# Performance work log

Measured on AMD Instinct MI355X. Metric: run time of the kernel, lower is better.

Reference implementation:

```python
import jax
import jax.numpy as jnp
import numpy as np

B, S, D, H, HID, E, TOPK = 1, 2048, 1024, 16, 4096, 8, 2
HEAD_DIM = D // H


def _layer_norm(x, g, b, eps=1e-5):
    mu = jnp.mean(x, axis=-1, keepdims=True)
    var = jnp.var(x, axis=-1, keepdims=True)
    return (x - mu) * jax.lax.rsqrt(var + eps) * g + b


def setup_inputs() -> dict:
    key = jax.random.key(0)
    ks = jax.random.split(key, 12)
    s = 0.02
    return {
        "x": jax.random.normal(ks[0], (B, S, D), jnp.float32),
        "ln1_g": jnp.ones((D,), jnp.float32),
        "ln1_b": jnp.zeros((D,), jnp.float32),
        "wq": jax.random.normal(ks[1], (D, D), jnp.float32) * s,
        "wk": jax.random.normal(ks[2], (D, D), jnp.float32) * s,
        "wv": jax.random.normal(ks[3], (D, D), jnp.float32) * s,
        "wo": jax.random.normal(ks[4], (D, D), jnp.float32) * s,
        "ln2_g": jnp.ones((D,), jnp.float32),
        "ln2_b": jnp.zeros((D,), jnp.float32),
        "w_gate": jax.random.normal(ks[5], (D, E), jnp.float32) * s,
        "w_eg": jax.random.normal(ks[6], (E, D, HID), jnp.float32) * s,
        "w_eu": jax.random.normal(ks[7], (E, D, HID), jnp.float32) * s,
        "w_ed": jax.random.normal(ks[8], (E, HID, D), jnp.float32) * s,
    }


def _attention(h, wq, wk, wv, wo):
    b, s, d = h.shape
    q = (h @ wq).reshape(b, s, H, HEAD_DIM).transpose(0, 2, 1, 3)
    k = (h @ wk).reshape(b, s, H, HEAD_DIM).transpose(0, 2, 1, 3)
    v = (h @ wv).reshape(b, s, H, HEAD_DIM).transpose(0, 2, 1, 3)
    scores = jnp.einsum("bhqd,bhkd->bhqk", q, k) / jnp.sqrt(jnp.asarray(HEAD_DIM, h.dtype))
    causal = jnp.tril(jnp.ones((s, s), bool))  # [s,s]
    scores = jnp.where(causal, scores, jnp.asarray(-1e30, h.dtype))
    attn = jax.nn.softmax(scores, axis=-1)
    out = jnp.einsum("bhqk,bhkd->bhqd", attn, v).transpose(0, 2, 1, 3).reshape(b, s, d)
    return out @ wo


def _moe(h, w_gate, w_eg, w_eu, w_ed):
    b, s, d = h.shape
    flat = h.reshape(-1, d)  # [T,D]
    logits = flat @ w_gate  # [T,E]
    scores = jax.nn.sigmoid(logits)
    top_val, top_idx = jax.lax.top_k(scores, TOPK)
    top_val = top_val / (jnp.sum(top_val, axis=-1, keepdims=True) + 1e-9)
    # per-token per-expert combine weight (0 for unrouted experts)
    combine = jnp.sum(jax.nn.one_hot(top_idx, E, dtype=flat.dtype) * top_val[..., None], axis=1)  # [T,E]
    g = jax.nn.silu(jnp.einsum("td,edh->eth", flat, w_eg))
    u = jnp.einsum("td,edh->eth", flat, w_eu)
    eo = jnp.einsum("eth,ehd->etd", g * u, w_ed)  # [E,T,D]
    out = jnp.einsum("etd,te->td", eo, combine)
    return out.reshape(b, s, d)


def reference(x, ln1_g, ln1_b, wq, wk, wv, wo, ln2_g, ln2_b, w_gate, w_eg, w_eu, w_ed):
    x = x + _attention(_layer_norm(x, ln1_g, ln1_b), wq, wk, wv, wo)
    x = x + _moe(_layer_norm(x, ln2_g, ln2_b), w_gate, w_eg, w_eu, w_ed)
    return x
```

## Files before the change

### kernel.cpp

```cpp
#include <hip/hip_runtime.h>
#include <hip/hip_bf16.h>
#include <stdint.h>

#define DI __device__ __forceinline__

typedef short bf16x8_t __attribute__((ext_vector_type(8)));
typedef float f32x4_t __attribute__((ext_vector_type(4)));

DI unsigned short f2bf(float f) {
  __hip_bfloat16 h = __float2bfloat16(f);
  unsigned short u;
  __builtin_memcpy(&u, &h, 2);
  return u;
}

DI uint32_t pk2(float a, float b) {
  return (uint32_t)f2bf(a) | ((uint32_t)f2bf(b) << 16);
}

DI f32x4_t mfma16(bf16x8_t a, bf16x8_t b, f32x4_t c) {
  return __builtin_amdgcn_mfma_f32_16x16x32_bf16(a, b, c, 0, 0, 0);
}

DI void gload16(const void* g, void* l) {
  __builtin_amdgcn_global_load_lds(
      (const __attribute__((address_space(1))) uint32_t*)g,
      (__attribute__((address_space(3))) uint32_t*)l, 16, 0, 0);
}

DI bf16x8_t frag(const unsigned short* base, int row, int hi) {
  return *(const bf16x8_t*)&base[row * 32 + ((hi ^ ((row >> 1) & 3)) * 8)];
}
DI int chunk_swz(int tid) { return ((tid & 3) ^ ((tid >> 3) & 3)) * 8; }

__global__ __launch_bounds__(256) void transpose_cvt4(const float* __restrict__ s0, const float* __restrict__ s1,
                                                      const float* __restrict__ s2, const float* __restrict__ s3,
                                                      unsigned short* __restrict__ d0, unsigned short* __restrict__ d1,
                                                      unsigned short* __restrict__ d2, unsigned short* __restrict__ d3) {
  __shared__ float tile[64][65];
  const int z = blockIdx.z;
  const float* in = (z == 0) ? s0 : (z == 1) ? s1 : (z == 2) ? s2 : s3;
  unsigned short* out = (z == 0) ? d0 : (z == 1) ? d1 : (z == 2) ? d2 : d3;
  const int tid = threadIdx.x;
  const int tx = tid & 15, ty = tid >> 4;
  const int r0 = blockIdx.y * 64, c0 = blockIdx.x * 64;
#pragma unroll
  for (int i = 0; i < 4; ++i) {
    const int r = ty + i * 16;
    const float4 v = *(const float4*)(in + (size_t)(r0 + r) * 1024 + c0 + tx * 4);
    tile[r][tx * 4 + 0] = v.x; tile[r][tx * 4 + 1] = v.y;
    tile[r][tx * 4 + 2] = v.z; tile[r][tx * 4 + 3] = v.w;
  }
  __syncthreads();
#pragma unroll
  for (int i = 0; i < 4; ++i) {
    const int r = ty + i * 16;
    ushort4 o;
    o.x = f2bf(tile[tx * 4 + 0][r]); o.y = f2bf(tile[tx * 4 + 1][r]);
    o.z = f2bf(tile[tx * 4 + 2][r]); o.w = f2bf(tile[tx * 4 + 3][r]);
    *(ushort4*)(out + (size_t)(c0 + r) * 1024 + r0 + tx * 4) = o;
  }
}

__global__ __launch_bounds__(256) void ln_kernel(const float* __restrict__ x, const float* __restrict__ g,
                                                 const float* __restrict__ b, unsigned short* __restrict__ out) {
  const int row = blockIdx.x, tid = threadIdx.x;
  const int wid = tid >> 6, lane = tid & 63;
  const float4 v = *(const float4*)(x + (size_t)row * 1024 + tid * 4);
  float s = v.x + v.y + v.z + v.w;
  float s2 = v.x * v.x + v.y * v.y + v.z * v.z + v.w * v.w;
#pragma unroll
  for (int o = 1; o < 64; o <<= 1) { s += __shfl_xor(s, o); s2 += __shfl_xor(s2, o); }
  __shared__ float red[8];
  if (lane == 0) { red[wid] = s; red[4 + wid] = s2; }
  __syncthreads();
  const float ts = red[0] + red[1] + red[2] + red[3];
  const float ts2 = red[4] + red[5] + red[6] + red[7];
  const float mu = ts * 0.0009765625f;
  const float var = ts2 * 0.0009765625f - mu * mu;
  const float rs = rsqrtf(var + 1e-5f);
  const float4 gg = *(const float4*)(g + tid * 4);
  const float4 bb = *(const float4*)(b + tid * 4);
  ushort4 o4;
  o4.x = f2bf((v.x - mu) * rs * gg.x + bb.x);
  o4.y = f2bf((v.y - mu) * rs * gg.y + bb.y);
  o4.z = f2bf((v.z - mu) * rs * gg.z + bb.z);
  o4.w = f2bf((v.w - mu) * rs * gg.w + bb.w);
  *(ushort4*)(out + (size_t)row * 1024 + tid * 4) = o4;
}

template<int BN>
DI void gemm_loop(const unsigned short* aR0, const unsigned short* aR1,
                  const unsigned short* bR0, const unsigned short* bR1,
                  const int K, unsigned short* lds, const int tid,
                  f32x4_t (&acc)[4][BN / 32]) {
  constexpr int NF = BN / 32;
  unsigned short* ldsA = lds;
  unsigned short* ldsB = lds + 4096;
  const int wid = tid >> 6, lane = tid & 63, ln = lane & 15, hi = lane >> 4;
  const int wr = wid >> 1, wc = wid & 1;
  char* dstA0 = (char*)ldsA + wid * 1024;
  char* dstA1 = (char*)ldsA + 4096 + wid * 1024;
  char* dstB0 = (char*)ldsB + wid * 1024;
  char* dstB1 = (char*)ldsB + 4096 + wid * 1024;
  for (int k0 = 0; k0 < K; k0 += 32) {
    gload16(aR0 + k0, dstA0);
    gload16(aR1 + k0, dstA1);
    gload16(bR0 + k0, dstB0);
    if constexpr (BN == 128) gload16(bR1 + k0, dstB1);
    __syncthreads();
    bf16x8_t af[4];
#pragma unroll
    for (int mf = 0; mf < 4; ++mf)
      af[mf] = frag(ldsA, wr * 64 + mf * 16 + ln, hi);
    __builtin_amdgcn_s_setprio(1);
#pragma unroll
    for (int nf = 0; nf < NF; ++nf) {
      bf16x8_t bfr = frag(ldsB, wc * (BN / 2) + nf * 16 + ln, hi);
#pragma unroll
      for (int mf = 0; mf < 4; ++mf)
        acc[mf][nf] = mfma16(af[mf], bfr, acc[mf][nf]);
    }
    __builtin_amdgcn_s_setprio(0);
    __syncthreads();
  }
}

__global__ __launch_bounds__(256) void qkv_kernel(const unsigned short* __restrict__ h1,
                                                  const unsigned short* __restrict__ wqT,
                                                  const unsigned short* __restrict__ wkT,
                                                  const unsigned short* __restrict__ wvT,
                                                  unsigned short* __restrict__ qb,
                                                  unsigned short* __restrict__ kbf,
                                                  unsigned short* __restrict__ vt) {
  __shared__ unsigned short lds[128 * 32 + 128 * 32];
  const int tid = threadIdx.x;
  const int z = blockIdx.z;
  const unsigned short* BT = (z == 0) ? wqT : (z == 1) ? wkT : wvT;
  const int m0 = blockIdx.y * 128, n0 = blockIdx.x * 128;
  f32x4_t acc[4][4] = {};
  const int cs = chunk_swz(tid);
  const unsigned short* aR0 = h1 + (size_t)(m0 + (tid >> 2)) * 1024 + cs;
  const unsigned short* aR1 = aR0 + 64 * 1024;
  const unsigned short* bR0 = BT + (size_t)(n0 + (tid >> 2)) * 1024 + cs;
  const unsigned short* bR1 = bR0 + 64 * 1024;
  gemm_loop<128>(aR0, aR1, bR0, bR1, 1024, lds, tid, acc);
  const int lane = tid & 63, ln = lane & 15, hi = lane >> 4, wid = tid >> 6;
  const int wr = wid >> 1, wc = wid & 1;
  if (z < 2) {
    unsigned short* o = z ? kbf : qb;
#pragma unroll
    for (int mf = 0; mf < 4; ++mf)
#pragma unroll
      for (int nf = 0; nf < 4; ++nf)
#pragma unroll
        for (int r = 0; r < 4; ++r) {
          const int m = m0 + wr * 64 + mf * 16 + hi * 4 + r;
          const int n = n0 + wc * 64 + nf * 16 + ln;
          o[(size_t)m * 1024 + n] = f2bf(acc[mf][nf][r]);
        }
  } else {
#pragma unroll
    for (int mf = 0; mf < 4; ++mf)
#pragma unroll
      for (int nf = 0; nf < 4; ++nf) {
        const int n = n0 + wc * 64 + nf * 16 + ln;
        const int mb = m0 + wr * 64 + mf * 16 + hi * 4;
        ushort4 o;
        o.x = f2bf(acc[mf][nf][0]); o.y = f2bf(acc[mf][nf][1]);
        o.z = f2bf(acc[mf][nf][2]); o.w = f2bf(acc[mf][nf][3]);
        *(ushort4*)(vt + (size_t)n * 2048 + mb) = o;
      }
  }
}

__global__ __launch_bounds__(256) void wo_kernel(const unsigned short* __restrict__ ao,
                                                 const unsigned short* __restrict__ woT,
                                                 const float* __restrict__ x,
                                                 float* __restrict__ out) {
  __shared__ unsigned short lds[128 * 32 + 64 * 32];
  const int tid = threadIdx.x;
  const int m0 = blockIdx.y * 128, n0 = blockIdx.x * 64;
  f32x4_t acc[4][2] = {};
  const int cs = chunk_swz(tid);
  const unsigned short* aR0 = ao + (size_t)(m0 + (tid >> 2)) * 1024 + cs;
  const unsigned short* aR1 = aR0 + 64 * 1024;
  const unsigned short* bR0 = woT + (size_t)(n0 + (tid >> 2)) * 1024 + cs;
  gemm_loop<64>(aR0, aR1, bR0, nullptr, 1024, lds, tid, acc);
  const int lane = tid & 63, ln = lane & 15, hi = lane >> 4, wid = tid >> 6;
  const int wr = wid >> 1, wc = wid & 1;
#pragma unroll
  for (int mf = 0; mf < 4; ++mf)
#pragma unroll
    for (int nf = 0; nf < 2; ++nf)
#pragma unroll
      for (int r = 0; r < 4; ++r) {
        const int m = m0 + wr * 64 + mf * 16 + hi * 4 + r;
        const int n = n0 + wc * 32 + nf * 16 + ln;
        out[(size_t)m * 1024 + n] = acc[mf][nf][r] + x[(size_t)m * 1024 + n];
      }
}

__global__ __launch_bounds__(256) void attn_kernel(const unsigned short* __restrict__ qb,
                                                   const unsigned short* __restrict__ kbuf,
                                                   const unsigned short* __restrict__ vt,
                                                   unsigned short* __restrict__ ao) {
  __shared__ unsigned short kTl[4096];
  __shared__ unsigned short vTl[4096];
  __shared__ unsigned short pl[4][1024];
  const int tid = threadIdx.x;
  const int wid = tid >> 6, lane = tid & 63;
  const int ln = lane & 15, hi = lane >> 4;
  const int h = blockIdx.y;
  const int qi = (h < 8) ? blockIdx.x : (31 - blockIdx.x);
  const int q0 = qi * 64;
  const int q0w = q0 + wid * 16;

  const unsigned short* qrow = qb + (size_t)(q0w + ln) * 1024 + h * 64 + hi * 8;
  const bf16x8_t aq0 = *(const bf16x8_t*)(qrow);
  const bf16x8_t aq1 = *(const bf16x8_t*)(qrow + 32);

  const int str_r = tid >> 3, str_c = tid & 7;
  const int swc = (str_c ^ (str_r & 7)) * 8;
  const unsigned short* ksrc0 = kbuf + (size_t)str_r * 1024 + h * 64 + swc;
  const unsigned short* ksrc1 = kbuf + (size_t)(str_r + 32) * 1024 + h * 64 + swc;
  const unsigned short* vsrc0 = vt + (size_t)(h * 64 + str_r) * 2048 + swc;
  const unsigned short* vsrc1 = vt + (size_t)(h * 64 + str_r + 32) * 2048 + swc;
  char* kd0 = (char*)kTl + wid * 1024;
  char* kd1 = (char*)kTl + 4096 + wid * 1024;
  char* vd0 = (char*)vTl + wid * 1024;
  char* vd1 = (char*)vTl + 4096 + wid * 1024;

  float m_r[4], l_r[4];
  f32x4_t o_acc[4] = {};
#pragma unroll
  for (int r = 0; r < 4; ++r) { m_r[r] = -1e30f; l_r[r] = 0.f; }

  const int nkv = qi + 1;
  for (int it = 0; it < nkv; ++it) {
    const int kv0 = it * 64;
    gload16(ksrc0 + (size_t)kv0 * 1024, kd0);
    gload16(ksrc1 + (size_t)kv0 * 1024, kd1);
    gload16(vsrc0 + kv0, vd0);
    gload16(vsrc1 + kv0, vd1);
    __syncthreads();

    float sc[4][4];
    __builtin_amdgcn_s_setprio(1);
#pragma unroll
    for (int cf = 0; cf < 4; ++cf) {
      const int row = cf * 16 + ln;
      const int swz = row & 7;
      const bf16x8_t b0 = *(const bf16x8_t*)((char*)kTl + row * 128 + ((hi ^ swz) * 16));
      const bf16x8_t b1 = *(const bf16x8_t*)((char*)kTl + row * 128 + (((4 + hi) ^ swz) * 16));
      f32x4_t zacc = {};
      zacc = mfma16(aq0, b0, zacc);
      zacc = mfma16(aq1, b1, zacc);
#pragma unroll
      for (int r = 0; r < 4; ++r) sc[cf][r] = zacc[r] * 0.125f;
    }
    __builtin_amdgcn_s_setprio(0);
    if (kv0 + 63 > q0w) {
#pragma unroll
      for (int cf = 0; cf < 4; ++cf)
#pragma unroll
        for (int r = 0; r < 4; ++r) {
          const int qg = q0w + hi * 4 + r;
          const int kg = kv0 + cf * 16 + ln;
          if (kg > qg) sc[cf][r] = -1e30f;
        }
    }
#pragma unroll
    for (int r = 0; r < 4; ++r) {
      float tm = fmaxf(fmaxf(sc[0][r], sc[1][r]), fmaxf(sc[2][r], sc[3][r]));
      tm = fmaxf(tm, __shfl_xor(tm, 1));
      tm = fmaxf(tm, __shfl_xor(tm, 2));
      tm = fmaxf(tm, __shfl_xor(tm, 4));
      tm = fmaxf(tm, __shfl_xor(tm, 8));
      const float mn = fmaxf(m_r[r], tm);
      const float alpha = __expf(m_r[r] - mn);
      float rsum = 0.f;
#pragma unroll
      for (int cf = 0; cf < 4; ++cf) {
        const float p = __expf(sc[cf][r] - mn);
        sc[cf][r] = p; rsum += p;
      }
      rsum += __shfl_xor(rsum, 1); rsum += __shfl_xor(rsum, 2);
      rsum += __shfl_xor(rsum, 4); rsum += __shfl_xor(rsum, 8);
      l_r[r] = l_r[r] * alpha + rsum;
      m_r[r] = mn;
#pragma unroll
      for (int df = 0; df < 4; ++df) o_acc[df][r] *= alpha;
    }
    unsigned short* pw = &pl[wid][0];
#pragma unroll
    for (int cf = 0; cf < 4; ++cf)
#pragma unroll
      for (int r = 0; r < 4; ++r) {
        const int qq = hi * 4 + r;
        const int kv = cf * 16 + ln;
        const int bo = (qq * 128 + kv * 2) ^ ((qq & 7) << 4);
        *(unsigned short*)((char*)pw + bo) = f2bf(sc[cf][r]);
      }
    asm volatile("s_waitcnt lgkmcnt(0)" ::: "memory");
    __builtin_amdgcn_sched_barrier(0);
    const bf16x8_t pa0 = *(const bf16x8_t*)((char*)pw + ((ln * 128 + hi * 16) ^ ((ln & 7) << 4)));
    const bf16x8_t pa1 = *(const bf16x8_t*)((char*)pw + ((ln * 128 + 64 + hi * 16) ^ ((ln & 7) << 4)));
    __builtin_amdgcn_s_setprio(1);
#pragma unroll
    for (int df = 0; df < 4; ++df) {
      const int d = df * 16 + ln;
      const int swz = d & 7;
      const bf16x8_t bv0 = *(const bf16x8_t*)((char*)vTl + d * 128 + ((hi ^ swz) * 16));
      const bf16x8_t bv1 = *(const bf16x8_t*)((char*)vTl + d * 128 + (((4 + hi) ^ swz) * 16));
      o_acc[df] = mfma16(pa0, bv0, o_acc[df]);
      o_acc[df] = mfma16(pa1, bv1, o_acc[df]);
    }
    __builtin_amdgcn_s_setprio(0);
    __syncthreads();
  }
#pragma unroll
  for (int df = 0; df < 4; ++df) {
    const int n = h * 64 + df * 16 + ln;
#pragma unroll
    for (int r = 0; r < 4; ++r) {
      const int m = q0w + hi * 4 + r;
      ao[(size_t)m * 1024 + n] = f2bf(o_acc[df][r] / l_r[r]);
    }
  }
}

__global__ __launch_bounds__(256) void gate_kernel(const float* __restrict__ x2, const float* __restrict__ g,
                                                   const float* __restrict__ b, const float* __restrict__ wg,
                                                   unsigned short* __restrict__ h2o,
                                                   int2* __restrict__ te, float2* __restrict__ tw,
                                                   int* __restrict__ cnt) {
  const int tid = threadIdx.x, wid = tid >> 6, lane = tid & 63;
  const int t = blockIdx.x * 4 + wid;
  const float* row = x2 + (size_t)t * 1024;
  float vv[16];
#pragma unroll
  for (int i = 0; i < 4; ++i) *(float4*)&vv[i * 4] = *(const float4*)(row + lane * 16 + i * 4);
  float s = 0.f, s2 = 0.f;
#pragma unroll
  for (int j = 0; j < 16; ++j) { s += vv[j]; s2 += vv[j] * vv[j]; }
#pragma unroll
  for (int o = 1; o < 64; o <<= 1) { s += __shfl_xor(s, o); s2 += __shfl_xor(s2, o); }
  const float mu = s * 0.0009765625f;
  const float var = s2 * 0.0009765625f - mu * mu;
  const float rs = rsqrtf(var + 1e-5f);
  float acc[8] = {0.f, 0.f, 0.f, 0.f, 0.f, 0.f, 0.f, 0.f};
  bf16x8_t o0, o1;
#pragma unroll
  for (int j = 0; j < 16; ++j) {
    const int d = lane * 16 + j;
    const float xv = (vv[j] - mu) * rs * g[d] + b[d];
    if (j < 8) o0[j] = (short)f2bf(xv); else o1[j - 8] = (short)f2bf(xv);
    const float4 w0 = *(const float4*)(wg + d * 8);
    const float4 w1 = *(const float4*)(wg + d * 8 + 4);
    acc[0] += xv * w0.x; acc[1] += xv * w0.y; acc[2] += xv * w0.z; acc[3] += xv * w0.w;
    acc[4] += xv * w1.x; acc[5] += xv * w1.y; acc[6] += xv * w1.z; acc[7] += xv * w1.w;
  }
  *(bf16x8_t*)(h2o + (size_t)t * 1024 + lane * 16) = o0;
  *(bf16x8_t*)(h2o + (size_t)t * 1024 + lane * 16 + 8) = o1;
#pragma unroll
  for (int o = 1; o < 64; o <<= 1) {
#pragma unroll
    for (int e = 0; e < 8; ++e) acc[e] += __shfl_xor(acc[e], o);
  }
  if (lane == 0) {
    float sg[8];
#pragma unroll
    for (int e = 0; e < 8; ++e) sg[e] = 1.f / (1.f + __expf(-acc[e]));
    int e0 = 0;
#pragma unroll
    for (int e = 1; e < 8; ++e) if (sg[e] > sg[e0]) e0 = e;
    int e1 = (e0 == 0) ? 1 : 0;
#pragma unroll
    for (int e = 0; e < 8; ++e) if (e != e0 && sg[e] > sg[e1]) e1 = e;
    const float v0 = sg[e0], v1 = sg[e1];
    const float inv = 1.f / (v0 + v1 + 1e-9f);
    te[t] = make_int2(e0, e1);
    tw[t] = make_float2(v0 * inv, v1 * inv);
    atomicAdd(&cnt[e0], 1);
    atomicAdd(&cnt[e1], 1);
  }
}

__global__ void zero_counters(int* p) { if (threadIdx.x < 8) p[threadIdx.x] = 0; }

__global__ __launch_bounds__(256) void g2_kernel(const int* __restrict__ cnt, int* __restrict__ slot_off,
                                                 int* __restrict__ tile_expert, int* __restrict__ tile_rowbase,
                                                 int* __restrict__ cursor, int* __restrict__ assign_token,
                                                 float* __restrict__ assign_w) {
  const int tid = threadIdx.x;
  for (int i = tid; i < 8192; i += 256) { assign_token[i] = -1; assign_w[i] = 0.f; }
  if (tid == 0) {
    int base = 0, tiles = 0;
    for (int e = 0; e < 8; ++e) {
      const int c = cnt[e];
      slot_off[e] = base;
      cursor[e] = 0;
      const int nt = (c + 255) >> 8;
      for (int i = 0; i < nt; ++i) {
        tile_expert[tiles] = e;
        tile_rowbase[tiles] = base + i * 256;
        ++tiles;
      }
      base += nt * 256;
    }
    for (; tiles < 40; ++tiles) tile_expert[tiles] = -1;
  }
}

__global__ __launch_bounds__(256) void g3_kernel(const int2* __restrict__ te, const float2* __restrict__ tw,
                                                 const int* __restrict__ slot_off, int* __restrict__ cursor,
                                                 int* __restrict__ assign_token, float* __restrict__ assign_w) {
  const int t = blockIdx.x * 256 + threadIdx.x;
  const int2 e = te[t];
  const float2 w = tw[t];
  const int s0 = slot_off[e.x] + atomicAdd(&cursor[e.x], 1);
  assign_token[s0] = t; assign_w[s0] = w.x;
  const int s1 = slot_off[e.y] + atomicAdd(&cursor[e.y], 1);
  assign_token[s1] = t; assign_w[s1] = w.y;
}

DI void stageA4(const unsigned short* a0, const unsigned short* a1,
                const unsigned short* a2, const unsigned short* a3,
                int koff, char* Ab, int wid) {
  gload16(a0 + koff, Ab + wid * 1024);
  gload16(a1 + koff, Ab + 4096 + wid * 1024);
  gload16(a2 + koff, Ab + 8192 + wid * 1024);
  gload16(a3 + koff, Ab + 12288 + wid * 1024);
}
DI void stageA2(const unsigned short* a0, const unsigned short* a1,
                int koff, char* Ab, int wid) {
  gload16(a0 + koff, Ab + wid * 1024);
  gload16(a1 + koff, Ab + 4096 + wid * 1024);
}

DI void ug_write_b(char* Bn, const int* boff, const float4& q0, const float4& q1,
                   const float4& q2, const float4& q3) {
  const float* q0p = (const float*)&q0; const float* q1p = (const float*)&q1;
  const float* q2p = (const float*)&q2; const float* q3p = (const float*)&q3;
#pragma unroll
  for (int i = 0; i < 4; ++i) {
    uint2 w;
    w.x = pk2(q0p[i], q1p[i]);
    w.y = pk2(q2p[i], q3p[i]);
    *(uint2*)(Bn + boff[i]) = w;
  }
}

DI void ug_mfma256(const unsigned short* A, const char* Bb, int wr, int wc, int ln, int hi,
                   f32x4_t (&accg)[8][2], f32x4_t (&accu)[8][2]) {
  bf16x8_t af[8];
#pragma unroll
  for (int mf = 0; mf < 8; ++mf)
    af[mf] = frag(A, wr * 128 + mf * 16 + ln, hi);
  __builtin_amdgcn_s_setprio(1);
#pragma unroll
  for (int nf = 0; nf < 2; ++nf) {
    const int nrow = wc * 32 + nf * 16 + ln;
    int bo = nrow * 64 + hi * 16;
    bo ^= ((nrow >> 2) & 7) << 4;
    const bf16x8_t bg = *(const bf16x8_t*)(Bb + bo);
    const bf16x8_t bu = *(const bf16x8_t*)(Bb + 4096 + bo);
#pragma unroll
    for (int mf = 0; mf < 8; ++mf) {
      accg[mf][nf] = mfma16(af[mf], bg, accg[mf][nf]);
      accu[mf][nf] = mfma16(af[mf], bu, accu[mf][nf]);
    }
  }
  __builtin_amdgcn_s_setprio(0);
}

__global__ __launch_bounds__(256, 2) void upgate_kernel(const unsigned short* __restrict__ h2,
                                                        const float* __restrict__ w_eg, const float* __restrict__ w_eu,
                                                        const int* __restrict__ tile_expert,
                                                        const int* __restrict__ tile_rowbase,
                                                        const int* __restrict__ assign_token,
                                                        unsigned short* __restrict__ act) {
  const int by = blockIdx.y;
  const int e = tile_expert[by];
  if (e < 0) return;
  const int n0 = blockIdx.x * 64;
  const int rowbase = tile_rowbase[by];
  const int tid = threadIdx.x;
  __shared__ unsigned short lds[2 * 8192 + 2 * 4096];
  char* A0 = (char*)lds;
  char* A1 = (char*)lds + 16384;
  char* B0 = (char*)lds + 32768;
  char* B1 = (char*)lds + 40960;
  const int wid = tid >> 6, lane = tid & 63, ln = lane & 15, hi = lane >> 4;
  const int wr = wid >> 1, wc = wid & 1;
  const int r0s = rowbase + (tid >> 2);
  int tk0 = assign_token[r0s];        tk0 = tk0 < 0 ? 0 : tk0;
  int tk1 = assign_token[r0s + 64];   tk1 = tk1 < 0 ? 0 : tk1;
  int tk2 = assign_token[r0s + 128];  tk2 = tk2 < 0 ? 0 : tk2;
  int tk3 = assign_token[r0s + 192];  tk3 = tk3 < 0 ? 0 : tk3;
  const int cs = chunk_swz(tid);
  const unsigned short* aR0 = h2 + (size_t)tk0 * 1024 + cs;
  const unsigned short* aR1 = h2 + (size_t)tk1 * 1024 + cs;
  const unsigned short* aR2 = h2 + (size_t)tk2 * 1024 + cs;
  const unsigned short* aR3 = h2 + (size_t)tk3 * 1024 + cs;
  const int mat = tid >> 7;
  const int blk = tid & 127;
  const int kb = (blk >> 4) * 4;
  const int nb = (blk & 15) * 4;
  const float* bsrc = (mat ? w_eu : w_eg) + (size_t)e * 1024 * 4096 + (size_t)kb * 4096 + n0 + nb;
  int boff[4];
#pragma unroll
  for (int i = 0; i < 4; ++i) {
    const int n = nb + i;
    int bo = mat * 4096 + n * 64 + kb * 2;
    bo ^= ((n >> 2) & 7) << 4;
    boff[i] = bo;
  }
  f32x4_t accg[8][2] = {};
  f32x4_t accu[8][2] = {};
  float4 qA0, qA1, qA2, qA3, qB0, qB1, qB2, qB3;
  stageA4(aR0, aR1, aR2, aR3, 0, A0, wid);
  qB0 = *(const float4*)(bsrc);
  qB1 = *(const float4*)(bsrc + 4096);
  qB2 = *(const float4*)(bsrc + 8192);
  qB3 = *(const float4*)(bsrc + 12288);
  __builtin_amdgcn_sched_barrier(0);
  ug_write_b(B0, boff, qB0, qB1, qB2, qB3);
  {
    const float* bs = bsrc + (size_t)32 * 4096;
    qA0 = *(const float4*)(bs);
    qA1 = *(const float4*)(bs + 4096);
    qA2 = *(const float4*)(bs + 8192);
    qA3 = *(const float4*)(bs + 12288);
  }
  asm volatile("s_waitcnt lgkmcnt(0)" ::: "memory");
  __builtin_amdgcn_sched_barrier(0);
  __builtin_amdgcn_s_barrier();
  for (int p = 0; p < 15; ++p) {
    {
      const int t = 2 * p;
      stageA4(aR0, aR1, aR2, aR3, (t + 1) * 32, A1, wid);
      const float* bs = bsrc + (size_t)(t + 2) * 32 * 4096;
      qB0 = *(const float4*)(bs);
      qB1 = *(const float4*)(bs + 4096);
      qB2 = *(const float4*)(bs + 8192);
      qB3 = *(const float4*)(bs + 12288);
      __builtin_amdgcn_sched_barrier(0);
      ug_write_b(B1, boff, qA0, qA1, qA2, qA3);
      ug_mfma256((const unsigned short*)A0, B0, wr, wc, ln, hi, accg, accu);
      asm volatile("s_waitcnt vmcnt(4)" ::: "memory");
      __builtin_amdgcn_sched_barrier(0);
      asm volatile("s_waitcnt lgkmcnt(0)" ::: "memory");
      __builtin_amdgcn_sched_barrier(0);
      __builtin_amdgcn_s_barrier();
    }
    {
      const int t = 2 * p + 1;
      stageA4(aR0, aR1, aR2, aR3, (t + 1) * 32, A0, wid);
      const float* bs = bsrc + (size_t)(t + 2) * 32 * 4096;
      qA0 = *(const float4*)(bs);
      qA1 = *(const float4*)(bs + 4096);
      qA2 = *(const float4*)(bs + 8192);
      qA3 = *(const float4*)(bs + 12288);
      __builtin_amdgcn_sched_barrier(0);
      ug_write_b(B0, boff, qB0, qB1, qB2, qB3);
      ug_mfma256((const unsigned short*)A1, B1, wr, wc, ln, hi, accg, accu);
      asm volatile("s_waitcnt vmcnt(4)" ::: "memory");
      __builtin_amdgcn_sched_barrier(0);
      asm volatile("s_waitcnt lgkmcnt(0)" ::: "memory");
      __builtin_amdgcn_sched_barrier(0);
      __builtin_amdgcn_s_barrier();
    }
  }
  stageA4(aR0, aR1, aR2, aR3, 31 * 32, A1, wid);
  __builtin_amdgcn_sched_barrier(0);
  ug_write_b(B1, boff, qA0, qA1, qA2, qA3);
  ug_mfma256((const unsigned short*)A0, B0, wr, wc, ln, hi, accg, accu);
  asm volatile("s_waitcnt vmcnt(0)" ::: "memory");
  __builtin_amdgcn_sched_barrier(0);
  asm volatile("s_waitcnt lgkmcnt(0)" ::: "memory");
  __builtin_amdgcn_sched_barrier(0);
  __builtin_amdgcn_s_barrier();
  ug_mfma256((const unsigned short*)A1, B1, wr, wc, ln, hi, accg, accu);
#pragma unroll
  for (int mf = 0; mf < 8; ++mf)
#pragma unroll
    for (int nf = 0; nf < 2; ++nf)
#pragma unroll
      for (int r = 0; r < 4; ++r) {
        const int m = wr * 128 + mf * 16 + hi * 4 + r;
        const int n = n0 + wc * 32 + nf * 16 + ln;
        const float gv = accg[mf][nf][r], uv = accu[mf][nf][r];
        const float val = gv / (1.f + __expf(-gv)) * uv;
        act[(size_t)(rowbase + m) * 4096 + n] = f2bf(val);
      }
}

DI void dn_write_b(char* Bn, const int* boff, const float4& q0, const float4& q1) {
  const float* q0p = (const float*)&q0; const float* q1p = (const float*)&q1;
#pragma unroll
  for (int i = 0; i < 4; ++i)
    *(uint32_t*)(Bn + boff[i]) = pk2(q0p[i], q1p[i]);
}

DI void dn_mfma(const unsigned short* A, const char* Bb, int wr, int wc, int ln, int hi,
                f32x4_t (&acc)[4][2]) {
  bf16x8_t af[4];
#pragma unroll
  for (int mf = 0; mf < 4; ++mf)
    af[mf] = frag(A, wr * 64 + mf * 16 + ln, hi);
  __builtin_amdgcn_s_setprio(1);
#pragma unroll
  for (int nf = 0; nf < 2; ++nf) {
    const int nrow = wc * 32 + nf * 16 + ln;
    int bo = nrow * 64 + hi * 16;
    bo ^= ((nrow >> 2) & 7) << 4;
    const bf16x8_t bb = *(const bf16x8_t*)(Bb + bo);
#pragma unroll
    for (int mf = 0; mf < 4; ++mf)
      acc[mf][nf] = mfma16(af[mf], bb, acc[mf][nf]);
  }
  __builtin_amdgcn_s_setprio(0);
}

__global__ __launch_bounds__(256) void down_kernel(const unsigned short* __restrict__ act,
                                                   const float* __restrict__ w_ed,
                                                   const int* __restrict__ tile_expert,
                                                   const int* __restrict__ tile_rowbase,
                                                   const int* __restrict__ assign_token,
                                                   const float* __restrict__ assign_w,
                                                   float* __restrict__ out) {
  const int tix = blockIdx.y;
  const int e = tile_expert[tix >> 1];
  if (e < 0) return;
  const int rowbase = tile_rowbase[tix >> 1] + (tix & 1) * 128;
  const int n0 = blockIdx.x * 64;
  const int kz = blockIdx.z * 1024;
  const int tid = threadIdx.x;
  __shared__ unsigned short lds[2 * 4096 + 2 * 2048];
  char* A0 = (char*)lds;
  char* A1 = (char*)lds + 8192;
  char* B0 = (char*)lds + 16384;
  char* B1 = (char*)lds + 20480;
  const int wid = tid >> 6, lane = tid & 63, ln = lane & 15, hi = lane >> 4;
  const int wr = wid >> 1, wc = wid & 1;
  const int cs = chunk_swz(tid);
  const unsigned short* aR0 = act + (size_t)(rowbase + (tid >> 2)) * 4096 + kz + cs;
  const unsigned short* aR1 = aR0 + (size_t)64 * 4096;
  const int nb = (tid & 15) * 4;
  const int kb2 = (tid >> 4) * 2;
  const float* bsrc = w_ed + (size_t)e * 4096 * 1024 + (size_t)(kz + kb2) * 1024 + n0 + nb;
  int boff[4];
#pragma unroll
  for (int i = 0; i < 4; ++i) {
    const int n = nb + i;
    int bo = n * 64 + kb2 * 2;
    bo ^= ((n >> 2) & 7) << 4;
    boff[i] = bo;
  }
  f32x4_t acc[4][2] = {};
  float4 qA0, qA1, qB0, qB1;
  stageA2(aR0, aR1, 0, A0, wid);
  qB0 = *(const float4*)(bsrc);
  qB1 = *(const float4*)(bsrc + 1024);
  __builtin_amdgcn_sched_barrier(0);
  dn_write_b(B0, boff, qB0, qB1);
  {
    const float* bs = bsrc + (size_t)32 * 1024;
    qA0 = *(const float4*)(bs);
    qA1 = *(const float4*)(bs + 1024);
  }
  asm volatile("s_waitcnt lgkmcnt(0)" ::: "memory");
  __builtin_amdgcn_sched_barrier(0);
  __builtin_amdgcn_s_barrier();
  for (int p = 0; p < 15; ++p) {
    {
      const int t = 2 * p;
      stageA2(aR0, aR1, (t + 1) * 32, A1, wid);
      const float* bs = bsrc + (size_t)(t + 2) * 32 * 1024;
      qB0 = *(const float4*)(bs);
      qB1 = *(const float4*)(bs + 1024);
      __builtin_amdgcn_sched_barrier(0);
      dn_write_b(B1, boff, qA0, qA1);
      dn_mfma((const unsigned short*)A0, B0, wr, wc, ln, hi, acc);
      asm volatile("s_waitcnt vmcnt(2)" ::: "memory");
      __builtin_amdgcn_sched_barrier(0);
      asm volatile("s_waitcnt lgkmcnt(0)" ::: "memory");
      __builtin_amdgcn_sched_barrier(0);
      __builtin_amdgcn_s_barrier();
    }
    {
      const int t = 2 * p + 1;
      stageA2(aR0, aR1, (t + 1) * 32, A0, wid);
      const float* bs = bsrc + (size_t)(t + 2) * 32 * 1024;
      qA0 = *(const float4*)(bs);
      qA1 = *(const float4*)(bs + 1024);
      __builtin_amdgcn_sched_barrier(0);
      dn_write_b(B0, boff, qB0, qB1);
      dn_mfma((const unsigned short*)A1, B1, wr, wc, ln, hi, acc);
      asm volatile("s_waitcnt vmcnt(2)" ::: "memory");
      __builtin_amdgcn_sched_barrier(0);
      asm volatile("s_waitcnt lgkmcnt(0)" ::: "memory");
      __builtin_amdgcn_sched_barrier(0);
      __builtin_amdgcn_s_barrier();
    }
  }
  stageA2(aR0, aR1, 31 * 32, A1, wid);
  __builtin_amdgcn_sched_barrier(0);
  dn_write_b(B1, boff, qA0, qA1);
  dn_mfma((const unsigned short*)A0, B0, wr, wc, ln, hi, acc);
  asm volatile("s_waitcnt vmcnt(0)" ::: "memory");
  __builtin_amdgcn_sched_barrier(0);
  asm volatile("s_waitcnt lgkmcnt(0)" ::: "memory");
  __builtin_amdgcn_sched_barrier(0);
  __builtin_amdgcn_s_barrier();
  dn_mfma((const unsigned short*)A1, B1, wr, wc, ln, hi, acc);
#pragma unroll
  for (int mf = 0; mf < 4; ++mf)
#pragma unroll
    for (int r = 0; r < 4; ++r) {
      const int m = wr * 64 + mf * 16 + hi * 4 + r;
      const int slot = rowbase + m;
      const int tk = assign_token[slot];
      if (tk >= 0) {
        const float w = assign_w[slot];
#pragma unroll
        for (int nf = 0; nf < 2; ++nf) {
          const int n = n0 + wc * 32 + nf * 16 + ln;
          atomicAdd(out + (size_t)tk * 1024 + n, acc[mf][nf][r] * w);
        }
      }
    }
}

extern "C" void kernel_launch(void* const* d_in, const int* in_sizes, int n_in,
                              void* d_out, int out_size, void* d_ws, size_t ws_size,
                              hipStream_t stream) {
  (void)in_sizes; (void)n_in; (void)out_size;
  const float* x    = (const float*)d_in[0];
  const float* ln1g = (const float*)d_in[1];
  const float* ln1b = (const float*)d_in[2];
  const float* wq   = (const float*)d_in[3];
  const float* wk   = (const float*)d_in[4];
  const float* wv   = (const float*)d_in[5];
  const float* wo   = (const float*)d_in[6];
  const float* ln2g = (const float*)d_in[7];
  const float* ln2b = (const float*)d_in[8];
  const float* wg   = (const float*)d_in[9];
  const float* weg  = (const float*)d_in[10];
  const float* weu  = (const float*)d_in[11];
  const float* wed  = (const float*)d_in[12];
  float* out = (float*)d_out;
  char* ws = (char*)d_ws;

  const size_t MB = (size_t)1 << 20;
  if (ws_size < 86 * MB) return;
  unsigned short* wqT = (unsigned short*)(ws + 0 * MB);
  unsigned short* wkT = (unsigned short*)(ws + 2 * MB);
  unsigned short* wvT = (unsigned short*)(ws + 4 * MB);
  unsigned short* woT = (unsigned short*)(ws + 6 * MB);
  unsigned short* h1  = (unsigned short*)(ws + 8 * MB);
  unsigned short* qb  = (unsigned short*)(ws + 12 * MB);
  unsigned short* kbf = (unsigned short*)(ws + 16 * MB);
  unsigned short* vt  = (unsigned short*)(ws + 20 * MB);
  unsigned short* ao  = (unsigned short*)(ws + 24 * MB);
  unsigned short* h2  = (unsigned short*)(ws + 28 * MB);
  unsigned short* act = (unsigned short*)(ws + 32 * MB);
  int2*   te = (int2*)(ws + 84 * MB);
  float2* tw = (float2*)(ws + 84 * MB + 16384);
  int*  meta = (int*)(ws + 84 * MB + 32768);
  int* cnt = meta;
  int* cursor = meta + 8;
  int* slot_off = meta + 16;
  int* tile_expert = meta + 24;
  int* tile_rowbase = meta + 64;
  int*   assign_token = (int*)(ws + 84 * MB + 36864);
  float* assign_w     = (float*)(ws + 84 * MB + 36864 + 32768);

  zero_counters<<<1, 64, 0, stream>>>(cnt);
  transpose_cvt4<<<dim3(16, 16, 4), 256, 0, stream>>>(wq, wk, wv, wo, wqT, wkT, wvT, woT);
  ln_kernel<<<2048, 256, 0, stream>>>(x, ln1g, ln1b, h1);
  qkv_kernel<<<dim3(8, 16, 3), 256, 0, stream>>>(h1, wqT, wkT, wvT, qb, kbf, vt);
  attn_kernel<<<dim3(32, 16), 256, 0, stream>>>(qb, kbf, vt, ao);
  wo_kernel<<<dim3(16, 16), 256, 0, stream>>>(ao, woT, x, out);
  gate_kernel<<<512, 256, 0, stream>>>(out, ln2g, ln2b, wg, h2, te, tw, cnt);
  g2_kernel<<<1, 256, 0, stream>>>(cnt, slot_off, tile_expert, tile_rowbase, cursor, assign_token, assign_w);
  g3_kernel<<<8, 256, 0, stream>>>(te, tw, slot_off, cursor, assign_token, assign_w);
  upgate_kernel<<<dim3(64, 24), 256, 0, stream>>>(h2, weg, weu, tile_expert, tile_rowbase, assign_token, act);
  down_kernel<<<dim3(16, 48, 4), 256, 0, stream>>>(act, wed, tile_expert, tile_rowbase, assign_token, assign_w, out);
}
```

Measured before the change: 481.2 us.

## Double-buffer LDS tiles in GEMM loop and attention KV loop

The GEMM main loop and the attention KV loop now use two LDS buffers. The next K-tile (or KV tile) is fetched from global memory while MFMAs run on the current one, and the barrier before compute is removed, leaving one barrier per iteration. The goal is to hide global-to-LDS load latency behind matrix math. The cost is double the LDS footprint per block, which can lower occupancy, especially for the attention kernel.

```diff
diff --git a/kernel.cpp b/kernel.cpp
--- a/kernel.cpp
+++ b/kernel.cpp
@@ -95,28 +95,40 @@
                   const int K, unsigned short* lds, const int tid,
                   f32x4_t (&acc)[4][BN / 32]) {
   constexpr int NF = BN / 32;
-  unsigned short* ldsA = lds;
-  unsigned short* ldsB = lds + 4096;
+  constexpr int BSZ = (BN == 128) ? 4096 : 2048;
   const int wid = tid >> 6, lane = tid & 63, ln = lane & 15, hi = lane >> 4;
   const int wr = wid >> 1, wc = wid & 1;
-  char* dstA0 = (char*)ldsA + wid * 1024;
-  char* dstA1 = (char*)ldsA + 4096 + wid * 1024;
-  char* dstB0 = (char*)ldsB + wid * 1024;
-  char* dstB1 = (char*)ldsB + 4096 + wid * 1024;
-  for (int k0 = 0; k0 < K; k0 += 32) {
-    gload16(aR0 + k0, dstA0);
-    gload16(aR1 + k0, dstA1);
-    gload16(bR0 + k0, dstB0);
-    if constexpr (BN == 128) gload16(bR1 + k0, dstB1);
-    __syncthreads();
+  const int nk = K >> 5;
+  {
+    char* Ab = (char*)lds;
+    char* Bb = (char*)lds + 16384;
+    gload16(aR0, Ab + wid * 1024);
+    gload16(aR1, Ab + 4096 + wid * 1024);
+    gload16(bR0, Bb + wid * 1024);
+    if constexpr (BN == 128) gload16(bR1, Bb + 4096 + wid * 1024);
+  }
+  __syncthreads();
+  for (int t = 0; t < nk; ++t) {
+    if (t + 1 < nk) {
+      const int k0 = (t + 1) << 5;
+      const int b = (t + 1) & 1;
+      char* Ab = (char*)lds + b * 8192;
+      char* Bb = (char*)lds + 16384 + b * (BSZ * 2);
+      gload16(aR0 + k0, Ab + wid * 1024);
+      gload16(aR1 + k0, Ab + 4096 + wid * 1024);
+      gload16(bR0 + k0, Bb + wid * 1024);
+      if constexpr (BN == 128) gload16(bR1 + k0, Bb + 4096 + wid * 1024);
+    }
+    const unsigned short* A = lds + (t & 1) * 4096;
+    const unsigned short* B = lds + 8192 + (t & 1) * BSZ;
     bf16x8_t af[4];
 #pragma unroll
     for (int mf = 0; mf < 4; ++mf)
-      af[mf] = frag(ldsA, wr * 64 + mf * 16 + ln, hi);
+      af[mf] = frag(A, wr * 64 + mf * 16 + ln, hi);
     __builtin_amdgcn_s_setprio(1);
 #pragma unroll
     for (int nf = 0; nf < NF; ++nf) {
-      bf16x8_t bfr = frag(ldsB, wc * (BN / 2) + nf * 16 + ln, hi);
+      bf16x8_t bfr = frag(B, wc * (BN / 2) + nf * 16 + ln, hi);
 #pragma unroll
       for (int mf = 0; mf < 4; ++mf)
         acc[mf][nf] = mfma16(af[mf], bfr, acc[mf][nf]);
@@ -133,7 +145,7 @@
                                                   unsigned short* __restrict__ qb,
                                                   unsigned short* __restrict__ kbf,
                                                   unsigned short* __restrict__ vt) {
-  __shared__ unsigned short lds[128 * 32 + 128 * 32];
+  __shared__ unsigned short lds[16384];
   const int tid = threadIdx.x;
   const int z = blockIdx.z;
   const unsigned short* BT = (z == 0) ? wqT : (z == 1) ? wkT : wvT;
@@ -178,7 +190,7 @@
                                                  const unsigned short* __restrict__ woT,
                                                  const float* __restrict__ x,
                                                  float* __restrict__ out) {
-  __shared__ unsigned short lds[128 * 32 + 64 * 32];
+  __shared__ unsigned short lds[12288];
   const int tid = threadIdx.x;
   const int m0 = blockIdx.y * 128, n0 = blockIdx.x * 64;
   f32x4_t acc[4][2] = {};
@@ -205,8 +217,8 @@
                                                    const unsigned short* __restrict__ kbuf,
                                                    const unsigned short* __restrict__ vt,
                                                    unsigned short* __restrict__ ao) {
-  __shared__ unsigned short kTl[4096];
-  __shared__ unsigned short vTl[4096];
+  __shared__ unsigned short kTl[8192];
+  __shared__ unsigned short vTl[8192];
   __shared__ unsigned short pl[4][1024];
   const int tid = threadIdx.x;
   const int wid = tid >> 6, lane = tid & 63;
@@ -226,10 +238,6 @@
   const unsigned short* ksrc1 = kbuf + (size_t)(str_r + 32) * 1024 + h * 64 + swc;
   const unsigned short* vsrc0 = vt + (size_t)(h * 64 + str_r) * 2048 + swc;
   const unsigned short* vsrc1 = vt + (size_t)(h * 64 + str_r + 32) * 2048 + swc;
-  char* kd0 = (char*)kTl + wid * 1024;
-  char* kd1 = (char*)kTl + 4096 + wid * 1024;
-  char* vd0 = (char*)vTl + wid * 1024;
-  char* vd1 = (char*)vTl + 4096 + wid * 1024;
 
   float m_r[4], l_r[4];
   f32x4_t o_acc[4] = {};
@@ -237,13 +245,29 @@
   for (int r = 0; r < 4; ++r) { m_r[r] = -1e30f; l_r[r] = 0.f; }
 
   const int nkv = qi + 1;
+  {
+    char* kd = (char*)kTl;
+    char* vd = (char*)vTl;
+    gload16(ksrc0, kd + wid * 1024);
+    gload16(ksrc1, kd + 4096 + wid * 1024);
+    gload16(vsrc0, vd + wid * 1024);
+    gload16(vsrc1, vd + 4096 + wid * 1024);
+  }
+  __syncthreads();
   for (int it = 0; it < nkv; ++it) {
+    if (it + 1 < nkv) {
+      const int kvn = (it + 1) * 64;
+      const int b = (it + 1) & 1;
+      char* kd = (char*)kTl + b * 8192;
+      char* vd = (char*)vTl + b * 8192;
+      gload16(ksrc0 + (size_t)kvn * 1024, kd + wid * 1024);
+      gload16(ksrc1 + (size_t)kvn * 1024, kd + 4096 + wid * 1024);
+      gload16(vsrc0 + kvn, vd + wid * 1024);
+      gload16(vsrc1 + kvn, vd + 4096 + wid * 1024);
+    }
     const int kv0 = it * 64;
-    gload16(ksrc0 + (size_t)kv0 * 1024, kd0);
-    gload16(ksrc1 + (size_t)kv0 * 1024, kd1);
-    gload16(vsrc0 + kv0, vd0);
-    gload16(vsrc1 + kv0, vd1);
-    __syncthreads();
+    const char* kT = (char*)kTl + (it & 1) * 8192;
+    const char* vT = (char*)vTl + (it & 1) * 8192;
 
     float sc[4][4];
     __builtin_amdgcn_s_setprio(1);
@@ -251,8 +275,8 @@
     for (int cf = 0; cf < 4; ++cf) {
       const int row = cf * 16 + ln;
       const int swz = row & 7;
-      const bf16x8_t b0 = *(const bf16x8_t*)((char*)kTl + row * 128 + ((hi ^ swz) * 16));
-      const bf16x8_t b1 = *(const bf16x8_t*)((char*)kTl + row * 128 + (((4 + hi) ^ swz) * 16));
+      const bf16x8_t b0 = *(const bf16x8_t*)(kT + row * 128 + ((hi ^ swz) * 16));
+      const bf16x8_t b1 = *(const bf16x8_t*)(kT + row * 128 + (((4 + hi) ^ swz) * 16));
       f32x4_t zacc = {};
       zacc = mfma16(aq0, b0, zacc);
       zacc = mfma16(aq1, b1, zacc);
@@ -311,8 +335,8 @@
     for (int df = 0; df < 4; ++df) {
       const int d = df * 16 + ln;
       const int swz = d & 7;
-      const bf16x8_t bv0 = *(const bf16x8_t*)((char*)vTl + d * 128 + ((hi ^ swz) * 16));
-      const bf16x8_t bv1 = *(const bf16x8_t*)((char*)vTl + d * 128 + (((4 + hi) ^ swz) * 16));
+      const bf16x8_t bv0 = *(const bf16x8_t*)(vT + d * 128 + ((hi ^ swz) * 16));
+      const bf16x8_t bv1 = *(const bf16x8_t*)(vT + d * 128 + (((4 + hi) ^ swz) * 16));
       o_acc[df] = mfma16(pa0, bv0, o_acc[df]);
       o_acc[df] = mfma16(pa1, bv1, o_acc[df]);
     }
```

After: 480.1 us. About the same (-0.2%).
